# Kernel tuning notes

Measured on AMD Instinct MI355X. Metric: run time of the kernel, lower is better.

Reference implementation:

```python
import jax, jax.numpy as jnp
import numpy as np

N_NODES = 40000
N_EDGES = 640000
IN_CH = 128
OUT_CH = 128
BN_EPS = 1e-5


def setup_inputs() -> dict:
    key = jax.random.key(0)
    ks = jax.random.split(key, 8)
    x = jax.random.normal(ks[0], (N_NODES, IN_CH), dtype=jnp.float32)
    edge_index = jax.random.randint(ks[1], (2, N_EDGES), 0, N_NODES, dtype=jnp.int64)
    s1 = 1.0 / np.sqrt(IN_CH)
    s2 = 1.0 / np.sqrt(OUT_CH)
    W1 = jax.random.uniform(ks[2], (OUT_CH, IN_CH), jnp.float32, -s1, s1)
    b1 = jax.random.uniform(ks[3], (OUT_CH,), jnp.float32, -s1, s1)
    gamma = jnp.ones((OUT_CH,), jnp.float32)
    beta = jnp.zeros((OUT_CH,), jnp.float32)
    W2 = jax.random.uniform(ks[4], (OUT_CH, OUT_CH), jnp.float32, -s2, s2)
    b2 = jax.random.uniform(ks[5], (OUT_CH,), jnp.float32, -s2, s2)
    eps = jnp.float32(0.0)
    return {"x": x, "edge_index": edge_index, "W1": W1, "b1": b1,
            "gamma": gamma, "beta": beta, "W2": W2, "b2": b2, "eps": eps}


def reference(x, edge_index, W1, b1, gamma, beta, W2, b2, eps):
    src, dst = edge_index[0], edge_index[1]
    # neighbor sum: agg[v] = sum_{(u,v) in E} x[u]
    agg = jax.ops.segment_sum(x[src], dst, num_segments=N_NODES)  # [N, in_ch]
    h = (1.0 + eps) * x + agg
    # Linear 1
    h = h @ W1.T + b1  # [N, out_ch]
    # BatchNorm1d (training mode: batch stats, biased variance)
    mu = jnp.mean(h, axis=0)
    var = jnp.var(h, axis=0)
    h = (h - mu) * jax.lax.rsqrt(var + BN_EPS) * gamma + beta
    # ReLU + Linear 2
    h = jnp.maximum(h, 0.0)
    return h @ W2.T + b2
```

## Files before the change

### kernel.cpp

```cpp
#include <hip/hip_runtime.h>

#define NN 40000
#define NE 640000
#define BN_EPS 1e-5f

typedef __attribute__((ext_vector_type(8))) short bf16x8;
typedef __attribute__((ext_vector_type(4))) float f32x4;
typedef unsigned int uint;
typedef unsigned short ushort;

__device__ __forceinline__ float blo(uint u) { return __uint_as_float(u << 16); }
__device__ __forceinline__ float bhi(uint u) { return __uint_as_float(u & 0xFFFF0000u); }
__device__ __forceinline__ uint bpack(float lo, float hi) {
    uint a = __float_as_uint(lo); a = (a + 0x7FFFu + ((a >> 16) & 1u)) >> 16;
    uint b = __float_as_uint(hi); b = (b + 0x7FFFu + ((b >> 16) & 1u)) & 0xFFFF0000u;
    return a | b;
}
__device__ __forceinline__ uint4 cvt8(const float4* f4, int i) {
    float4 p = f4[i * 2], q = f4[i * 2 + 1];
    uint4 o;
    o.x = bpack(p.x, p.y); o.y = bpack(p.z, p.w);
    o.z = bpack(q.x, q.y); o.w = bpack(q.z, q.w);
    return o;
}

__global__ __launch_bounds__(256) void k_pre(const float* __restrict__ x, const float* __restrict__ W1,
                                             int* __restrict__ cnt, float* __restrict__ bn,
                                             uint* __restrict__ xb, uint* __restrict__ w1b) {
    int b = blockIdx.x, t = threadIdx.x;
    if (b < 157) {
        int i = b * 256 + t;
        if (i < NN) cnt[i] = 0;
        if (b == 156) bn[t] = 0.f;
    } else if (b < 2657) {
        int i = (b - 157) * 256 + t;
        ((uint4*)xb)[i] = cvt8((const float4*)x, i);
    } else {
        int i = (b - 2657) * 256 + t;
        ((uint4*)w1b)[i] = cvt8((const float4*)W1, i);
    }
}

__global__ __launch_bounds__(256) void k_bucket(const int* __restrict__ ei, int* __restrict__ cnt,
                                                ushort* __restrict__ srcl) {
    int e = blockIdx.x * 256 + threadIdx.x;
    if (e >= NE) return;
    int s = ei[e];
    int d = ei[NE + e];
    int pos = atomicAdd(&cnt[d], 1);
    if (pos < 64) srcl[d * 64 + pos] = (ushort)s;
}

__global__ __launch_bounds__(256) void k_gather(const uint* __restrict__ xbv, const int* __restrict__ cnt,
                                                const ushort* __restrict__ srcl, const float* __restrict__ epsp,
                                                uint* __restrict__ hb) {
    int wid = blockIdx.x * 4 + (threadIdx.x >> 6);
    int lane = threadIdx.x & 63;
    int deg = cnt[wid]; deg = deg > 64 ? 64 : deg;
    int sv = srcl[wid * 64 + lane];
    uint su = xbv[wid * 64 + lane];
    float e1 = 1.f + epsp[0];
    float a0 = blo(su) * e1, a1 = bhi(su) * e1;
    float c0 = 0.f, c1 = 0.f;
    int full = deg & ~7;
    for (int i = 0; i < full; i += 8) {
        int s0 = __builtin_amdgcn_readlane(sv, i);
        int s1 = __builtin_amdgcn_readlane(sv, i + 1);
        int s2 = __builtin_amdgcn_readlane(sv, i + 2);
        int s3 = __builtin_amdgcn_readlane(sv, i + 3);
        int s4 = __builtin_amdgcn_readlane(sv, i + 4);
        int s5 = __builtin_amdgcn_readlane(sv, i + 5);
        int s6 = __builtin_amdgcn_readlane(sv, i + 6);
        int s7 = __builtin_amdgcn_readlane(sv, i + 7);
        uint v0 = xbv[(size_t)s0 * 64 + lane];
        uint v1 = xbv[(size_t)s1 * 64 + lane];
        uint v2 = xbv[(size_t)s2 * 64 + lane];
        uint v3 = xbv[(size_t)s3 * 64 + lane];
        uint v4 = xbv[(size_t)s4 * 64 + lane];
        uint v5 = xbv[(size_t)s5 * 64 + lane];
        uint v6 = xbv[(size_t)s6 * 64 + lane];
        uint v7 = xbv[(size_t)s7 * 64 + lane];
        a0 += blo(v0) + blo(v1) + blo(v2) + blo(v3);
        c0 += blo(v4) + blo(v5) + blo(v6) + blo(v7);
        a1 += bhi(v0) + bhi(v1) + bhi(v2) + bhi(v3);
        c1 += bhi(v4) + bhi(v5) + bhi(v6) + bhi(v7);
    }
    if (deg & 7) {
#pragma unroll
        for (int j = 0; j < 8; ++j) {
            int idx = full + j;
            int s = __builtin_amdgcn_readlane(sv, idx);
            bool ok = idx < deg;
            s = ok ? s : 0;
            uint v = xbv[(size_t)s * 64 + lane];
            a0 += ok ? blo(v) : 0.f;
            a1 += ok ? bhi(v) : 0.f;
        }
    }
    hb[wid * 64 + lane] = bpack(a0 + c0, a1 + c1);
}

__global__ __launch_bounds__(256) void k_mm1(const ushort* __restrict__ hb, const ushort* __restrict__ w1b,
                                             const float* __restrict__ b1, float* __restrict__ h1,
                                             float* __restrict__ bnsum, float* __restrict__ bnsumsq) {
    __shared__ float rs[256 * 8];
    __shared__ float rq[256 * 8];
    const int tid = threadIdx.x;
    const int wave = tid >> 6;
    const int lane = tid & 63;
    const int lr = lane & 15;
    const int lk = lane >> 4;
    const int r0 = (blockIdx.x * 4 + wave) * 16;

    bf16x8 a[4];
#pragma unroll
    for (int ks = 0; ks < 4; ++ks)
        a[ks] = *reinterpret_cast<const bf16x8*>(&hb[(size_t)(r0 + lr) * 128 + ks * 32 + lk * 8]);

    f32x4 acc[8];
#pragma unroll
    for (int t = 0; t < 8; ++t) { acc[t][0] = 0.f; acc[t][1] = 0.f; acc[t][2] = 0.f; acc[t][3] = 0.f; }

#pragma unroll
    for (int t = 0; t < 8; ++t) {
        const ushort* wrow = &w1b[(size_t)(t * 16 + lr) * 128];
#pragma unroll
        for (int ks = 0; ks < 4; ++ks) {
            bf16x8 bfr = *reinterpret_cast<const bf16x8*>(&wrow[ks * 32 + lk * 8]);
            acc[t] = __builtin_amdgcn_mfma_f32_16x16x32_bf16(a[ks], bfr, acc[t], 0, 0, 0);
        }
    }
#pragma unroll
    for (int t = 0; t < 8; ++t) {
        float bias = b1[t * 16 + lr];
        float s = 0.f, q = 0.f;
#pragma unroll
        for (int i = 0; i < 4; ++i) {
            float v = acc[t][i] + bias;
            h1[(size_t)(r0 + lk * 4 + i) * 128 + t * 16 + lr] = v;
            s += v; q += v * v;
        }
        rs[tid * 8 + t] = s;
        rq[tid * 8 + t] = q;
    }
    __syncthreads();
    if (tid < 128) {
        int c = tid, t = c >> 4, cr = c & 15;
        float s = 0.f, q = 0.f;
#pragma unroll
        for (int w = 0; w < 4; ++w)
#pragma unroll
            for (int g = 0; g < 4; ++g) {
                int src = w * 64 + g * 16 + cr;
                s += rs[src * 8 + t];
                q += rq[src * 8 + t];
            }
        atomicAdd(&bnsum[c], s);
        atomicAdd(&bnsumsq[c], q);
    }
}

__global__ void k_bnfin(const float* __restrict__ bnsum, const float* __restrict__ bnsumsq,
                        const float* __restrict__ gamma, const float* __restrict__ beta,
                        float* __restrict__ scale, float* __restrict__ shift) {
    int c = threadIdx.x;
    if (c < 128) {
        float mu = bnsum[c] * (1.0f / NN);
        float var = bnsumsq[c] * (1.0f / NN) - mu * mu;
        float rs = rsqrtf(var + BN_EPS);
        float g = rs * gamma[c];
        scale[c] = g;
        shift[c] = beta[c] - mu * g;
    }
}

__global__ __launch_bounds__(256) void k_gemm2(const float* __restrict__ A, const float* __restrict__ W,
                                               const float* __restrict__ bias, float* __restrict__ out,
                                               const float* __restrict__ scale, const float* __restrict__ shift) {
    __shared__ float sA[64 * 65];
    __shared__ float sW[128 * 65];
    const int tid = threadIdx.x;
    const int tx = tid & 15;
    const int ty = tid >> 4;
    const int rb = blockIdx.x * 64;

    float acc[4][8];
#pragma unroll
    for (int i = 0; i < 4; ++i)
#pragma unroll
        for (int j = 0; j < 8; ++j) acc[i][j] = 0.f;

    for (int kb = 0; kb < 128; kb += 64) {
        __syncthreads();
#pragma unroll
        for (int it = 0; it < 4; ++it) {
            int idx = it * 256 + tid;
            int r = idx >> 4;
            int kq = idx & 15;
            float4 v = *(const float4*)&A[(size_t)(rb + r) * 128 + kb + kq * 4];
            float4 sc = *(const float4*)&scale[kb + kq * 4];
            float4 sh = *(const float4*)&shift[kb + kq * 4];
            v.x = fmaxf(0.f, fmaf(v.x, sc.x, sh.x));
            v.y = fmaxf(0.f, fmaf(v.y, sc.y, sh.y));
            v.z = fmaxf(0.f, fmaf(v.z, sc.z, sh.z));
            v.w = fmaxf(0.f, fmaf(v.w, sc.w, sh.w));
            float* d = &sA[r * 65 + kq * 4];
            d[0] = v.x; d[1] = v.y; d[2] = v.z; d[3] = v.w;
        }
#pragma unroll
        for (int it = 0; it < 8; ++it) {
            int idx = it * 256 + tid;
            int c = idx >> 4;
            int kq = idx & 15;
            float4 v = *(const float4*)&W[c * 128 + kb + kq * 4];
            float* d = &sW[c * 65 + kq * 4];
            d[0] = v.x; d[1] = v.y; d[2] = v.z; d[3] = v.w;
        }
        __syncthreads();
#pragma unroll 4
        for (int k = 0; k < 64; ++k) {
            float a[4], w[8];
#pragma unroll
            for (int i = 0; i < 4; ++i) a[i] = sA[(ty * 4 + i) * 65 + k];
#pragma unroll
            for (int j = 0; j < 4; ++j) {
                w[j]     = sW[(tx * 4 + j) * 65 + k];
                w[j + 4] = sW[(tx * 4 + 64 + j) * 65 + k];
            }
#pragma unroll
            for (int i = 0; i < 4; ++i)
#pragma unroll
                for (int j = 0; j < 8; ++j)
                    acc[i][j] = fmaf(a[i], w[j], acc[i][j]);
        }
    }

    const int c0 = tx * 4, c1 = tx * 4 + 64;
    float4 b0 = *(const float4*)&bias[c0];
    float4 b1v = *(const float4*)&bias[c1];
#pragma unroll
    for (int i = 0; i < 4; ++i) {
        int row = rb + ty * 4 + i;
        float4 v0, v1;
        v0.x = acc[i][0] + b0.x;  v0.y = acc[i][1] + b0.y;  v0.z = acc[i][2] + b0.z;  v0.w = acc[i][3] + b0.w;
        v1.x = acc[i][4] + b1v.x; v1.y = acc[i][5] + b1v.y; v1.z = acc[i][6] + b1v.z; v1.w = acc[i][7] + b1v.w;
        *(float4*)&out[(size_t)row * 128 + c0] = v0;
        *(float4*)&out[(size_t)row * 128 + c1] = v1;
    }
}

extern "C" void kernel_launch(void* const* d_in, const int* in_sizes, int n_in,
                              void* d_out, int out_size, void* d_ws, size_t ws_size,
                              hipStream_t stream) {
    const float* x     = (const float*)d_in[0];
    const int*   ei    = (const int*)d_in[1];
    const float* W1    = (const float*)d_in[2];
    const float* b1    = (const float*)d_in[3];
    const float* gamma = (const float*)d_in[4];
    const float* beta  = (const float*)d_in[5];
    const float* W2    = (const float*)d_in[6];
    const float* b2    = (const float*)d_in[7];
    const float* eps   = (const float*)d_in[8];

    char* ws = (char*)d_ws;
    int*    cnt  = (int*)(ws + 0);
    ushort* srcl = (ushort*)(ws + 196608);
    uint*   xb   = (uint*)(ws + 5373952);
    uint*   hb   = (uint*)(ws + 15728640);
    uint*   w1b  = (uint*)(ws + 26083328);
    float*  bn   = (float*)(ws + 26148864);
    float* bnsum   = bn;
    float* bnsumsq = bn + 128;
    float* scale   = bn + 256;
    float* shift   = bn + 384;
    float* h1      = (float*)d_out;

    k_pre<<<2665, 256, 0, stream>>>(x, W1, cnt, bn, xb, w1b);
    k_bucket<<<2500, 256, 0, stream>>>(ei, cnt, srcl);
    k_gather<<<10000, 256, 0, stream>>>(xb, cnt, srcl, eps, hb);
    k_mm1<<<625, 256, 0, stream>>>((const ushort*)hb, (const ushort*)w1b, b1, h1, bnsum, bnsumsq);
    k_bnfin<<<1, 128, 0, stream>>>(bnsum, bnsumsq, gamma, beta, scale, shift);
    k_gemm2<<<625, 256, 0, stream>>>(h1, W2, b2, (float*)d_out, scale, shift);
}
```

Before: 123.5 us.

## Move second GEMM to bf16 MFMA and fold BN finalize into it

Replaces the fp32 shared-memory SIMT second GEMM with a bf16 MFMA kernel that mirrors the first GEMM. The first GEMM now stores its intermediate in bf16, halving that buffer's write and read traffic, and W2 is converted to bf16 in the pre-pass. The one-block BN finalize kernel is removed and each block recomputes scale and shift, which drops one launch. This costs extra rounding on the intermediate activations and on W2.

```diff
diff --git a/kernel.cpp b/kernel.cpp
--- a/kernel.cpp
+++ b/kernel.cpp
@@ -16,6 +16,9 @@
     uint b = __float_as_uint(hi); b = (b + 0x7FFFu + ((b >> 16) & 1u)) & 0xFFFF0000u;
     return a | b;
 }
+__device__ __forceinline__ ushort b1pack(float v) {
+    uint u = __float_as_uint(v); return (ushort)((u + 0x7FFFu + ((u >> 16) & 1u)) >> 16);
+}
 __device__ __forceinline__ uint4 cvt8(const float4* f4, int i) {
     float4 p = f4[i * 2], q = f4[i * 2 + 1];
     uint4 o;
@@ -25,8 +28,10 @@
 }
 
 __global__ __launch_bounds__(256) void k_pre(const float* __restrict__ x, const float* __restrict__ W1,
+                                             const float* __restrict__ W2,
                                              int* __restrict__ cnt, float* __restrict__ bn,
-                                             uint* __restrict__ xb, uint* __restrict__ w1b) {
+                                             uint* __restrict__ xb, uint* __restrict__ w1b,
+                                             uint* __restrict__ w2b) {
     int b = blockIdx.x, t = threadIdx.x;
     if (b < 157) {
         int i = b * 256 + t;
@@ -35,9 +40,12 @@
     } else if (b < 2657) {
         int i = (b - 157) * 256 + t;
         ((uint4*)xb)[i] = cvt8((const float4*)x, i);
-    } else {
+    } else if (b < 2665) {
         int i = (b - 2657) * 256 + t;
         ((uint4*)w1b)[i] = cvt8((const float4*)W1, i);
+    } else {
+        int i = (b - 2665) * 256 + t;
+        ((uint4*)w2b)[i] = cvt8((const float4*)W2, i);
     }
 }
 
@@ -101,7 +109,7 @@
 }
 
 __global__ __launch_bounds__(256) void k_mm1(const ushort* __restrict__ hb, const ushort* __restrict__ w1b,
-                                             const float* __restrict__ b1, float* __restrict__ h1,
+                                             const float* __restrict__ b1, ushort* __restrict__ h1b,
                                              float* __restrict__ bnsum, float* __restrict__ bnsumsq) {
     __shared__ float rs[256 * 8];
     __shared__ float rq[256 * 8];
@@ -137,7 +145,7 @@
 #pragma unroll
         for (int i = 0; i < 4; ++i) {
             float v = acc[t][i] + bias;
-            h1[(size_t)(r0 + lk * 4 + i) * 128 + t * 16 + lr] = v;
+            h1b[(size_t)(r0 + lk * 4 + i) * 128 + t * 16 + lr] = b1pack(v);
             s += v; q += v * v;
         }
         rs[tid * 8 + t] = s;
@@ -160,92 +168,63 @@
     }
 }
 
-__global__ void k_bnfin(const float* __restrict__ bnsum, const float* __restrict__ bnsumsq,
-                        const float* __restrict__ gamma, const float* __restrict__ beta,
-                        float* __restrict__ scale, float* __restrict__ shift) {
-    int c = threadIdx.x;
-    if (c < 128) {
-        float mu = bnsum[c] * (1.0f / NN);
-        float var = bnsumsq[c] * (1.0f / NN) - mu * mu;
-        float rs = rsqrtf(var + BN_EPS);
-        float g = rs * gamma[c];
-        scale[c] = g;
-        shift[c] = beta[c] - mu * g;
-    }
-}
-
-__global__ __launch_bounds__(256) void k_gemm2(const float* __restrict__ A, const float* __restrict__ W,
-                                               const float* __restrict__ bias, float* __restrict__ out,
-                                               const float* __restrict__ scale, const float* __restrict__ shift) {
-    __shared__ float sA[64 * 65];
-    __shared__ float sW[128 * 65];
+__global__ __launch_bounds__(256) void k_mm2(const ushort* __restrict__ h1b, const ushort* __restrict__ w2b,
+                                             const float* __restrict__ b2,
+                                             const float* __restrict__ bnsum, const float* __restrict__ bnsumsq,
+                                             const float* __restrict__ gamma, const float* __restrict__ beta,
+                                             float* __restrict__ out) {
+    __shared__ float ssc[128], ssh[128];
     const int tid = threadIdx.x;
-    const int tx = tid & 15;
-    const int ty = tid >> 4;
-    const int rb = blockIdx.x * 64;
-
-    float acc[4][8];
-#pragma unroll
-    for (int i = 0; i < 4; ++i)
-#pragma unroll
-        for (int j = 0; j < 8; ++j) acc[i][j] = 0.f;
-
-    for (int kb = 0; kb < 128; kb += 64) {
-        __syncthreads();
-#pragma unroll
-        for (int it = 0; it < 4; ++it) {
-            int idx = it * 256 + tid;
-            int r = idx >> 4;
-            int kq = idx & 15;
-            float4 v = *(const float4*)&A[(size_t)(rb + r) * 128 + kb + kq * 4];
-            float4 sc = *(const float4*)&scale[kb + kq * 4];
-            float4 sh = *(const float4*)&shift[kb + kq * 4];
-            v.x = fmaxf(0.f, fmaf(v.x, sc.x, sh.x));
-            v.y = fmaxf(0.f, fmaf(v.y, sc.y, sh.y));
-            v.z = fmaxf(0.f, fmaf(v.z, sc.z, sh.z));
-            v.w = fmaxf(0.f, fmaf(v.w, sc.w, sh.w));
-            float* d = &sA[r * 65 + kq * 4];
-            d[0] = v.x; d[1] = v.y; d[2] = v.z; d[3] = v.w;
-        }
-#pragma unroll
-        for (int it = 0; it < 8; ++it) {
-            int idx = it * 256 + tid;
-            int c = idx >> 4;
-            int kq = idx & 15;
-            float4 v = *(const float4*)&W[c * 128 + kb + kq * 4];
-            float* d = &sW[c * 65 + kq * 4];
-            d[0] = v.x; d[1] = v.y; d[2] = v.z; d[3] = v.w;
-        }
-        __syncthreads();
-#pragma unroll 4
-        for (int k = 0; k < 64; ++k) {
-            float a[4], w[8];
-#pragma unroll
-            for (int i = 0; i < 4; ++i) a[i] = sA[(ty * 4 + i) * 65 + k];
-#pragma unroll
-            for (int j = 0; j < 4; ++j) {
-                w[j]     = sW[(tx * 4 + j) * 65 + k];
-                w[j + 4] = sW[(tx * 4 + 64 + j) * 65 + k];
-            }
-#pragma unroll
-            for (int i = 0; i < 4; ++i)
-#pragma unroll
-                for (int j = 0; j < 8; ++j)
-                    acc[i][j] = fmaf(a[i], w[j], acc[i][j]);
-        }
-    }
-
-    const int c0 = tx * 4, c1 = tx * 4 + 64;
-    float4 b0 = *(const float4*)&bias[c0];
-    float4 b1v = *(const float4*)&bias[c1];
-#pragma unroll
-    for (int i = 0; i < 4; ++i) {
-        int row = rb + ty * 4 + i;
-        float4 v0, v1;
-        v0.x = acc[i][0] + b0.x;  v0.y = acc[i][1] + b0.y;  v0.z = acc[i][2] + b0.z;  v0.w = acc[i][3] + b0.w;
-        v1.x = acc[i][4] + b1v.x; v1.y = acc[i][5] + b1v.y; v1.z = acc[i][6] + b1v.z; v1.w = acc[i][7] + b1v.w;
-        *(float4*)&out[(size_t)row * 128 + c0] = v0;
-        *(float4*)&out[(size_t)row * 128 + c1] = v1;
+    if (tid < 128) {
+        float mu = bnsum[tid] * (1.0f / NN);
+        float var = bnsumsq[tid] * (1.0f / NN) - mu * mu;
+        float rsv = rsqrtf(var + BN_EPS);
+        float g = rsv * gamma[tid];
+        ssc[tid] = g;
+        ssh[tid] = beta[tid] - mu * g;
+    }
+    __syncthreads();
+
+    const int wave = tid >> 6;
+    const int lane = tid & 63;
+    const int lr = lane & 15;
+    const int lk = lane >> 4;
+    const int r0 = (blockIdx.x * 4 + wave) * 16;
+
+    bf16x8 a[4];
+#pragma unroll
+    for (int ks = 0; ks < 4; ++ks) {
+        int kbase = ks * 32 + lk * 8;
+        bf16x8 raw = *reinterpret_cast<const bf16x8*>(&h1b[(size_t)(r0 + lr) * 128 + kbase]);
+        bf16x8 o;
+#pragma unroll
+        for (int j = 0; j < 8; ++j) {
+            float v = __uint_as_float(((uint)(ushort)raw[j]) << 16);
+            v = fmaxf(0.f, fmaf(v, ssc[kbase + j], ssh[kbase + j]));
+            o[j] = (short)b1pack(v);
+        }
+        a[ks] = o;
+    }
+
+    f32x4 acc[8];
+#pragma unroll
+    for (int t = 0; t < 8; ++t) { acc[t][0] = 0.f; acc[t][1] = 0.f; acc[t][2] = 0.f; acc[t][3] = 0.f; }
+
+#pragma unroll
+    for (int t = 0; t < 8; ++t) {
+        const ushort* wrow = &w2b[(size_t)(t * 16 + lr) * 128];
+#pragma unroll
+        for (int ks = 0; ks < 4; ++ks) {
+            bf16x8 bfr = *reinterpret_cast<const bf16x8*>(&wrow[ks * 32 + lk * 8]);
+            acc[t] = __builtin_amdgcn_mfma_f32_16x16x32_bf16(a[ks], bfr, acc[t], 0, 0, 0);
+        }
+    }
+#pragma unroll
+    for (int t = 0; t < 8; ++t) {
+        float bias = b2[t * 16 + lr];
+#pragma unroll
+        for (int i = 0; i < 4; ++i)
+            out[(size_t)(r0 + lk * 4 + i) * 128 + t * 16 + lr] = acc[t][i] + bias;
     }
 }
 
@@ -267,18 +246,16 @@
     ushort* srcl = (ushort*)(ws + 196608);
     uint*   xb   = (uint*)(ws + 5373952);
     uint*   hb   = (uint*)(ws + 15728640);
-    uint*   w1b  = (uint*)(ws + 26083328);
-    float*  bn   = (float*)(ws + 26148864);
+    ushort* h1b  = (ushort*)(ws + 26083328);
+    uint*   w1b  = (uint*)(ws + 36438016);
+    uint*   w2b  = (uint*)(ws + 36503552);
+    float*  bn   = (float*)(ws + 36569088);
     float* bnsum   = bn;
     float* bnsumsq = bn + 128;
-    float* scale   = bn + 256;
-    float* shift   = bn + 384;
-    float* h1      = (float*)d_out;
-
-    k_pre<<<2665, 256, 0, stream>>>(x, W1, cnt, bn, xb, w1b);
+
+    k_pre<<<2673, 256, 0, stream>>>(x, W1, W2, cnt, bn, xb, w1b, w2b);
     k_bucket<<<2500, 256, 0, stream>>>(ei, cnt, srcl);
     k_gather<<<10000, 256, 0, stream>>>(xb, cnt, srcl, eps, hb);
-    k_mm1<<<625, 256, 0, stream>>>((const ushort*)hb, (const ushort*)w1b, b1, h1, bnsum, bnsumsq);
-    k_bnfin<<<1, 128, 0, stream>>>(bnsum, bnsumsq, gamma, beta, scale, shift);
-    k_gemm2<<<625, 256, 0, stream>>>(h1, W2, b2, (float*)d_out, scale, shift);
-}
+    k_mm1<<<625, 256, 0, stream>>>((const ushort*)hb, (const ushort*)w1b, b1, h1b, bnsum, bnsumsq);
+    k_mm2<<<625, 256, 0, stream>>>(h1b, (const ushort*)w2b, b2, bnsum, bnsumsq, gamma, beta, (float*)d_out);
+}
```

Measured after the change: 107.7 us. 1.15x faster.
